# Optimization experiments

Measured on AMD Instinct MI355X. Metric: run time of the kernel, lower is better.

## Reference

```python
import jax, jax.numpy as jnp
import numpy as np

NUM_CLASSES = 21
THRESHOLD = 0.5
NEGPOS_RATIO = 3
VAR0, VAR1 = 0.1, 0.2


def setup_inputs() -> dict:
    key = jax.random.key(0)
    k1, k2, k3, k4, k5, k6, k7 = jax.random.split(key, 7)
    N, P, M = 64, 24564, 16
    loc_data = jax.random.normal(k1, (N, P, 4), dtype=jnp.float32)
    conf_data = jax.random.normal(k2, (N, P, NUM_CLASSES), dtype=jnp.float32)
    # priors in center form (cx, cy, w, h), all inside the unit square
    pc = jax.random.uniform(k3, (P, 2)) * 0.9 + 0.05
    pwh = jax.random.uniform(k4, (P, 2)) * 0.2 + 0.02
    priors = jnp.concatenate([pc, pwh], axis=-1).astype(jnp.float32)
    # ground truth boxes in corner form (xmin, ymin, xmax, ymax, label)
    tc = jax.random.uniform(k5, (N, M, 2)) * 0.8 + 0.1
    twh = jax.random.uniform(k6, (N, M, 2)) * 0.2 + 0.05
    lab = jax.random.randint(k7, (N, M, 1), 0, NUM_CLASSES - 1).astype(jnp.float32)
    targets = jnp.concatenate([tc - twh / 2, tc + twh / 2, lab], axis=-1)
    return {"loc_data": loc_data, "conf_data": conf_data, "priors": priors, "targets": targets}


def _point_form(p):  # center form -> corner form
    return jnp.concatenate([p[:, :2] - p[:, 2:] / 2, p[:, :2] + p[:, 2:] / 2], axis=-1)


def _jaccard(a, b):  # a: [M,4] corner, b: [P,4] corner -> [M,P]
    max_xy = jnp.minimum(a[:, None, 2:], b[None, :, 2:])
    min_xy = jnp.maximum(a[:, None, :2], b[None, :, :2])
    inter = jnp.clip(max_xy - min_xy, 0.0).prod(-1)
    area_a = ((a[:, 2] - a[:, 0]) * (a[:, 3] - a[:, 1]))[:, None]
    area_b = ((b[:, 2] - b[:, 0]) * (b[:, 3] - b[:, 1]))[None, :]
    return inter / (area_a + area_b - inter)


def _encode(matched, priors):  # matched corner form [P,4], priors center form [P,4]
    g_cxcy = ((matched[:, :2] + matched[:, 2:]) / 2 - priors[:, :2]) / (VAR0 * priors[:, 2:])
    g_wh = jnp.log((matched[:, 2:] - matched[:, :2]) / priors[:, 2:]) / VAR1
    return jnp.concatenate([g_cxcy, g_wh], axis=-1)


def _match(truth, label, priors):  # truth [M,4], label [M], priors [P,4]
    overlaps = _jaccard(truth, _point_form(priors))        # [M,P]
    best_prior_idx = jnp.argmax(overlaps, axis=1)          # [M]
    best_truth_idx = jnp.argmax(overlaps, axis=0)          # [P]
    best_truth_ov = overlaps.max(axis=0)                   # [P]
    # ensure every gt matches its best prior
    best_truth_ov = best_truth_ov.at[best_prior_idx].set(2.0)
    best_truth_idx = best_truth_idx.at[best_prior_idx].set(jnp.arange(truth.shape[0]))
    matched = truth[best_truth_idx]                        # [P,4]
    conf = (label[best_truth_idx] + 1).astype(jnp.int32)
    conf = jnp.where(best_truth_ov < THRESHOLD, 0, conf)
    return _encode(matched, priors), conf


def _multibox_loss(loc_data, conf_data, priors, targets):
    truths, labels = targets[..., :4], targets[..., 4]
    loc_t, conf_t = jax.vmap(_match, in_axes=(0, 0, None))(truths, labels, priors)
    pos = conf_t > 0                                        # [N,P]

    # localization: smooth-L1, summed over positive priors
    diff = loc_data - loc_t
    adiff = jnp.abs(diff)
    sl1 = jnp.where(adiff < 1.0, 0.5 * diff * diff, adiff - 0.5)
    loss_l = jnp.sum(sl1 * pos[..., None].astype(sl1.dtype))

    # per-prior softmax CE loss for hard negative mining
    lse = jax.scipy.special.logsumexp(conf_data, axis=-1)   # [N,P]
    gathered = jnp.take_along_axis(conf_data, conf_t[..., None], axis=-1)[..., 0]
    loss_c_all = lse - gathered                             # [N,P]
    loss_c_mined = jnp.where(pos, 0.0, loss_c_all)
    loss_idx = jnp.argsort(-loss_c_mined, axis=1)
    idx_rank = jnp.argsort(loss_idx, axis=1)                # rank of each prior by loss
    num_pos = pos.sum(axis=1, keepdims=True)                # [N,1]
    num_neg = jnp.minimum(NEGPOS_RATIO * num_pos, pos.shape[1] - 1)
    neg = idx_rank < num_neg
    sel = pos | neg
    loss_c = jnp.sum(jnp.where(sel, loss_c_all, 0.0))

    n = num_pos.sum().astype(jnp.float32)
    return loss_l / n, loss_c / n


def reference(loc_data, conf_data, priors, targets):
    return _multibox_loss(loc_data, conf_data, priors, targets)
```

## Files before the change

### kernel.cpp

```cpp
#include <hip/hip_runtime.h>
#include <math.h>

constexpr int N = 64;
constexpr int P = 24564;
constexpr int M = 16;
constexpr int C = 21;
constexpr float THRESH = 0.5f;

constexpr size_t OFF_SLL  = 0;
constexpr size_t OFF_SPOS = OFF_SLL + (size_t)N * 4;
constexpr size_t OFF_NP   = OFF_SPOS + (size_t)N * 4;
constexpr size_t OFF_BPK  = ((OFF_NP + (size_t)N * 4 + 15) / 16) * 16;
constexpr size_t OFF_ZEND = OFF_BPK + (size_t)N * M * 8;
constexpr size_t OFF_LCROW = ((OFF_ZEND + 15) / 16) * 16;
constexpr size_t OFF_MINED = ((OFF_LCROW + (size_t)N * 4 + 15) / 16) * 16;
constexpr size_t WS_NEEDED = OFF_MINED + (size_t)N * P * 4;

__device__ __forceinline__ float smooth_l1(float d) {
    float a = fabsf(d);
    return (a < 1.0f) ? 0.5f * d * d : (a - 0.5f);
}

__global__ __launch_bounds__(256) void k_match(
    const float* __restrict__ priors, const float* __restrict__ targets,
    unsigned long long* __restrict__ bpk) {
    const int n = blockIdx.y;
    const int tid = threadIdx.x;
    const int p = blockIdx.x * 256 + tid;
    __shared__ float st[M * 5];
    __shared__ unsigned int sbp_ov[M];
    __shared__ unsigned int sbp_idx[M];
    if (tid < M * 5) st[tid] = targets[(size_t)n * M * 5 + tid];
    if (tid < M) { sbp_ov[tid] = 0u; sbp_idx[tid] = 0xFFFFFFFFu; }
    __syncthreads();

    const bool active = p < P;
    float ovs[M];
    if (active) {
        float4 pr = reinterpret_cast<const float4*>(priors)[p];
        float bx1 = pr.x - pr.z * 0.5f, by1 = pr.y - pr.w * 0.5f;
        float bx2 = pr.x + pr.z * 0.5f, by2 = pr.y + pr.w * 0.5f;
        float area_b = (bx2 - bx1) * (by2 - by1);
        #pragma unroll
        for (int m = 0; m < M; ++m) {
            float tx1 = st[m * 5 + 0], ty1 = st[m * 5 + 1];
            float tx2 = st[m * 5 + 2], ty2 = st[m * 5 + 3];
            float ix = fmaxf(fminf(tx2, bx2) - fmaxf(tx1, bx1), 0.0f);
            float iy = fmaxf(fminf(ty2, by2) - fmaxf(ty1, by1), 0.0f);
            float inter = ix * iy;
            float area_a = (tx2 - tx1) * (ty2 - ty1);
            float ov = inter / (area_a + area_b - inter);
            ovs[m] = ov;
            unsigned int bits = __float_as_uint(ov);
            if (bits > sbp_ov[m]) atomicMax(&sbp_ov[m], bits);
        }
    }
    __syncthreads();
    if (active) {
        #pragma unroll
        for (int m = 0; m < M; ++m) {
            if (__float_as_uint(ovs[m]) == sbp_ov[m])
                atomicMin(&sbp_idx[m], (unsigned)p);
        }
    }
    __syncthreads();
    if (tid < M) {
        unsigned long long key =
            ((unsigned long long)sbp_ov[tid] << 32) |
            (unsigned long long)(0xFFFFFFFFu - sbp_idx[tid]);
        unsigned long long* dst = &bpk[(size_t)n * M + tid];
        if (key > *dst) atomicMax(dst, key);
    }
}

__global__ __launch_bounds__(256) void k_loss(
    const float* __restrict__ loc, const float* __restrict__ conf,
    const float* __restrict__ priors, const float* __restrict__ targets,
    const unsigned long long* __restrict__ bpk,
    float* __restrict__ mined, float* __restrict__ s_ll,
    int* __restrict__ num_pos, float* __restrict__ s_pos) {
    const int n = blockIdx.y;
    const int p0 = blockIdx.x * 256;
    const int tid = threadIdx.x;
    __shared__ __align__(16) float sc[256 * C];
    __shared__ float st[M * 5];
    __shared__ unsigned int fprior[M];
    __shared__ float wll[4], wsp[4];
    __shared__ int wnp[4];

    {
        const float4* src4 = reinterpret_cast<const float4*>(
            conf + (size_t)n * P * C + (size_t)p0 * C);
        float4* sc4 = reinterpret_cast<float4*>(sc);
        int cnt4 = (min(256, P - p0) * C) >> 2;
        for (int i = tid; i < cnt4; i += 256) sc4[i] = src4[i];
    }
    if (tid < M * 5) st[tid] = targets[(size_t)n * M * 5 + tid];
    if (tid < M)
        fprior[tid] = 0xFFFFFFFFu -
                      (unsigned int)(bpk[(size_t)n * M + tid] & 0xFFFFFFFFull);
    __syncthreads();

    float my_ll = 0.0f, my_sp = 0.0f;
    int my_np = 0;
    const int p = p0 + tid;
    if (p < P) {
        float4 pr = reinterpret_cast<const float4*>(priors)[p];
        float bx1 = pr.x - pr.z * 0.5f, by1 = pr.y - pr.w * 0.5f;
        float bx2 = pr.x + pr.z * 0.5f, by2 = pr.y + pr.w * 0.5f;
        float area_b = (bx2 - bx1) * (by2 - by1);
        float bestv = -1.0f;
        int bestm = 0;
        #pragma unroll
        for (int m = 0; m < M; ++m) {
            float tx1 = st[m * 5 + 0], ty1 = st[m * 5 + 1];
            float tx2 = st[m * 5 + 2], ty2 = st[m * 5 + 3];
            float ix = fmaxf(fminf(tx2, bx2) - fmaxf(tx1, bx1), 0.0f);
            float iy = fmaxf(fminf(ty2, by2) - fmaxf(ty1, by1), 0.0f);
            float inter = ix * iy;
            float area_a = (tx2 - tx1) * (ty2 - ty1);
            float ov = inter / (area_a + area_b - inter);
            if (ov > bestv) { bestv = ov; bestm = m; }
        }
        #pragma unroll
        for (int m = 0; m < M; ++m) {
            if (fprior[m] == (unsigned)p) { bestv = 2.0f; bestm = m; }
        }
        bool pos = !(bestv < THRESH);
        float mx1 = st[bestm * 5 + 0], my1 = st[bestm * 5 + 1];
        float mx2 = st[bestm * 5 + 2], my2 = st[bestm * 5 + 3];
        int conf_t = pos ? ((int)st[bestm * 5 + 4] + 1) : 0;

        if (pos) {
            float gcx = ((mx1 + mx2) * 0.5f - pr.x) / (0.1f * pr.z);
            float gcy = ((my1 + my2) * 0.5f - pr.y) / (0.1f * pr.w);
            float gw = logf((mx2 - mx1) / pr.z) / 0.2f;
            float gh = logf((my2 - my1) / pr.w) / 0.2f;
            float4 ld = reinterpret_cast<const float4*>(loc)[(size_t)n * P + p];
            my_ll = smooth_l1(ld.x - gcx) + smooth_l1(ld.y - gcy) +
                    smooth_l1(ld.z - gw) + smooth_l1(ld.w - gh);
            my_np = 1;
        }
        float cv[C];
        #pragma unroll
        for (int c = 0; c < C; ++c) cv[c] = sc[tid * C + c];
        float mx = cv[0];
        #pragma unroll
        for (int c = 1; c < C; ++c) mx = fmaxf(mx, cv[c]);
        float s = 0.0f;
        #pragma unroll
        for (int c = 0; c < C; ++c) s += expf(cv[c] - mx);
        float gathered = sc[tid * C + conf_t];
        float lc = mx + logf(s) - gathered;
        if (pos) my_sp = lc;
        mined[(size_t)n * P + p] = pos ? 0.0f : lc;
    }

    for (int off = 32; off > 0; off >>= 1) {
        my_ll += __shfl_down(my_ll, off);
        my_sp += __shfl_down(my_sp, off);
        my_np += __shfl_down(my_np, off);
    }
    int wave = tid >> 6, lane = tid & 63;
    if (lane == 0) { wll[wave] = my_ll; wsp[wave] = my_sp; wnp[wave] = my_np; }
    __syncthreads();
    if (tid == 0) {
        float ll = wll[0] + wll[1] + wll[2] + wll[3];
        float sp = wsp[0] + wsp[1] + wsp[2] + wsp[3];
        int np_ = wnp[0] + wnp[1] + wnp[2] + wnp[3];
        if (ll != 0.0f) atomicAdd(&s_ll[n], ll);
        if (np_) atomicAdd(&num_pos[n], np_);
        if (sp != 0.0f) atomicAdd(&s_pos[n], sp);
    }
}

__global__ __launch_bounds__(1024) void k_select(
    const float* __restrict__ mined, const int* __restrict__ num_pos,
    const float* __restrict__ s_pos, float* __restrict__ lcrow) {
    const int n = blockIdx.x;
    const int tid = threadIdx.x;
    const int wid = tid >> 6, lane = tid & 63;
    const float4* row4 = reinterpret_cast<const float4*>(mined + (size_t)n * P);
    constexpr int P4 = P / 4;

    __shared__ unsigned int whist[16 * 256];
    __shared__ unsigned int hist[256];
    __shared__ unsigned int suf[256];
    __shared__ unsigned int s_prefix;
    __shared__ int s_remK;
    __shared__ float wsg[16];
    __shared__ int wcg[16];

    const int K = min(3 * num_pos[n], P - 1);
    if (K <= 0) {
        if (tid == 0) lcrow[n] = s_pos[n];
        return;
    }

    unsigned int prefix = 0;
    int remK = K;
    for (int pass = 0; pass < 4; ++pass) {
        const int shift = 24 - pass * 8;
        const unsigned int himask = (pass == 0) ? 0u : (0xFFFFFFFFu << (shift + 8));
        for (int i = tid; i < 16 * 256; i += 1024) whist[i] = 0;
        __syncthreads();
        unsigned int* mh = &whist[wid * 256];
        for (int i = tid; i < P4; i += 1024) {
            float4 v = row4[i];
            unsigned int k0 = __float_as_uint(v.x), k1 = __float_as_uint(v.y);
            unsigned int k2 = __float_as_uint(v.z), k3 = __float_as_uint(v.w);
            if ((k0 & himask) == prefix) atomicAdd(&mh[(k0 >> shift) & 255u], 1u);
            if ((k1 & himask) == prefix) atomicAdd(&mh[(k1 >> shift) & 255u], 1u);
            if ((k2 & himask) == prefix) atomicAdd(&mh[(k2 >> shift) & 255u], 1u);
            if ((k3 & himask) == prefix) atomicAdd(&mh[(k3 >> shift) & 255u], 1u);
        }
        __syncthreads();
        if (tid < 256) {
            unsigned int h = 0;
            #pragma unroll
            for (int w = 0; w < 16; ++w) h += whist[w * 256 + tid];
            hist[tid] = h;
        }
        __syncthreads();
        if (tid < 64) {
            unsigned int h0 = hist[tid * 4 + 0], h1 = hist[tid * 4 + 1];
            unsigned int h2 = hist[tid * 4 + 2], h3 = hist[tid * 4 + 3];
            unsigned int s3 = h3, s2 = h2 + s3, s1 = h1 + s2, s0 = h0 + s1;
            unsigned int tot = s0;
            #pragma unroll
            for (int off = 1; off < 64; off <<= 1) {
                unsigned int v = __shfl_down(tot, off);
                if (lane + off < 64) tot += v;
            }
            unsigned int above = tot - s0;
            suf[tid * 4 + 0] = above + s0;
            suf[tid * 4 + 1] = above + s1;
            suf[tid * 4 + 2] = above + s2;
            suf[tid * 4 + 3] = above + s3;
        }
        __syncthreads();
        if (tid < 256) {
            unsigned int Sb = suf[tid];
            unsigned int Sb1 = (tid == 255) ? 0u : suf[tid + 1];
            if (Sb >= (unsigned)remK && Sb1 < (unsigned)remK) {
                s_prefix = prefix | ((unsigned)tid << shift);
                s_remK = remK - (int)Sb1;
            }
        }
        __syncthreads();
        prefix = s_prefix;
        remK = s_remK;
        __syncthreads();
    }
    const float T = __uint_as_float(prefix);
    float sgt = 0.0f;
    int cgt = 0;
    for (int i = tid; i < P4; i += 1024) {
        float4 v = row4[i];
        if (v.x > T) { sgt += v.x; cgt++; }
        if (v.y > T) { sgt += v.y; cgt++; }
        if (v.z > T) { sgt += v.z; cgt++; }
        if (v.w > T) { sgt += v.w; cgt++; }
    }
    for (int off = 32; off > 0; off >>= 1) {
        sgt += __shfl_down(sgt, off);
        cgt += __shfl_down(cgt, off);
    }
    if (lane == 0) { wsg[wid] = sgt; wcg[wid] = cgt; }
    __syncthreads();
    if (tid == 0) {
        float S = 0.0f;
        int Cg = 0;
        #pragma unroll
        for (int w = 0; w < 16; ++w) { S += wsg[w]; Cg += wcg[w]; }
        lcrow[n] = s_pos[n] + S + (float)(K - Cg) * T;
    }
}

__global__ void k_final(const float* __restrict__ s_ll,
                        const int* __restrict__ num_pos,
                        const float* __restrict__ lcrow,
                        float* __restrict__ out) {
    int t = threadIdx.x;
    float llv = s_ll[t];
    int npv = num_pos[t];
    float lcv = lcrow[t];
    for (int off = 32; off > 0; off >>= 1) {
        llv += __shfl_down(llv, off);
        npv += __shfl_down(npv, off);
        lcv += __shfl_down(lcv, off);
    }
    if (t == 0) {
        float nf = (float)npv;
        out[0] = llv / nf;
        out[1] = lcv / nf;
    }
}

extern "C" void kernel_launch(void* const* d_in, const int* in_sizes, int n_in,
                              void* d_out, int out_size, void* d_ws, size_t ws_size,
                              hipStream_t stream) {
    const float* loc = (const float*)d_in[0];
    const float* conf = (const float*)d_in[1];
    const float* priors = (const float*)d_in[2];
    const float* targets = (const float*)d_in[3];

    if (ws_size < WS_NEEDED) return;

    char* ws = (char*)d_ws;
    float* s_ll = (float*)(ws + OFF_SLL);
    float* s_pos = (float*)(ws + OFF_SPOS);
    int* num_pos = (int*)(ws + OFF_NP);
    unsigned long long* bpk = (unsigned long long*)(ws + OFF_BPK);
    float* lcrow = (float*)(ws + OFF_LCROW);
    float* mined = (float*)(ws + OFF_MINED);

    hipMemsetAsync(ws, 0, OFF_ZEND, stream);

    dim3 grid((P + 255) / 256, N);
    k_match<<<grid, 256, 0, stream>>>(priors, targets, bpk);
    k_loss<<<grid, 256, 0, stream>>>(loc, conf, priors, targets, bpk,
                                     mined, s_ll, num_pos, s_pos);
    k_select<<<N, 1024, 0, stream>>>(mined, num_pos, s_pos, lcrow);
    k_final<<<1, 64, 0, stream>>>(s_ll, num_pos, lcrow, (float*)d_out);
}
```

Measured before the change: 318.0 us.

## Use wave-sized blocks, wave-level argmax, fast math, and two-stage candidate radix select

```diff
diff --git a/kernel.cpp b/kernel.cpp
--- a/kernel.cpp
+++ b/kernel.cpp
@@ -5,7 +5,6 @@
 constexpr int P = 24564;
 constexpr int M = 16;
 constexpr int C = 21;
-constexpr float THRESH = 0.5f;
 
 constexpr size_t OFF_SLL  = 0;
 constexpr size_t OFF_SPOS = OFF_SLL + (size_t)N * 4;
@@ -21,90 +20,76 @@
     return (a < 1.0f) ? 0.5f * d * d : (a - 0.5f);
 }
 
-__global__ __launch_bounds__(256) void k_match(
+__global__ __launch_bounds__(64) void k_match(
     const float* __restrict__ priors, const float* __restrict__ targets,
     unsigned long long* __restrict__ bpk) {
     const int n = blockIdx.y;
-    const int tid = threadIdx.x;
-    const int p = blockIdx.x * 256 + tid;
-    __shared__ float st[M * 5];
-    __shared__ unsigned int sbp_ov[M];
-    __shared__ unsigned int sbp_idx[M];
-    if (tid < M * 5) st[tid] = targets[(size_t)n * M * 5 + tid];
-    if (tid < M) { sbp_ov[tid] = 0u; sbp_idx[tid] = 0xFFFFFFFFu; }
-    __syncthreads();
-
+    const int lane = threadIdx.x;
+    const int p = blockIdx.x * 64 + lane;
     const bool active = p < P;
-    float ovs[M];
-    if (active) {
-        float4 pr = reinterpret_cast<const float4*>(priors)[p];
-        float bx1 = pr.x - pr.z * 0.5f, by1 = pr.y - pr.w * 0.5f;
-        float bx2 = pr.x + pr.z * 0.5f, by2 = pr.y + pr.w * 0.5f;
-        float area_b = (bx2 - bx1) * (by2 - by1);
-        #pragma unroll
-        for (int m = 0; m < M; ++m) {
-            float tx1 = st[m * 5 + 0], ty1 = st[m * 5 + 1];
-            float tx2 = st[m * 5 + 2], ty2 = st[m * 5 + 3];
-            float ix = fmaxf(fminf(tx2, bx2) - fmaxf(tx1, bx1), 0.0f);
-            float iy = fmaxf(fminf(ty2, by2) - fmaxf(ty1, by1), 0.0f);
-            float inter = ix * iy;
-            float area_a = (tx2 - tx1) * (ty2 - ty1);
-            float ov = inter / (area_a + area_b - inter);
-            ovs[m] = ov;
-            unsigned int bits = __float_as_uint(ov);
-            if (bits > sbp_ov[m]) atomicMax(&sbp_ov[m], bits);
-        }
-    }
-    __syncthreads();
-    if (active) {
-        #pragma unroll
-        for (int m = 0; m < M; ++m) {
-            if (__float_as_uint(ovs[m]) == sbp_ov[m])
-                atomicMin(&sbp_idx[m], (unsigned)p);
-        }
-    }
-    __syncthreads();
-    if (tid < M) {
-        unsigned long long key =
-            ((unsigned long long)sbp_ov[tid] << 32) |
-            (unsigned long long)(0xFFFFFFFFu - sbp_idx[tid]);
-        unsigned long long* dst = &bpk[(size_t)n * M + tid];
-        if (key > *dst) atomicMax(dst, key);
-    }
-}
-
-__global__ __launch_bounds__(256) void k_loss(
+    const float* tgt = targets + (size_t)n * M * 5;
+    const unsigned long long* bpk_row = bpk + (size_t)n * M;
+
+    float4 pr = reinterpret_cast<const float4*>(priors)[active ? p : (P - 1)];
+    float bx1 = pr.x - pr.z * 0.5f, by1 = pr.y - pr.w * 0.5f;
+    float bx2 = pr.x + pr.z * 0.5f, by2 = pr.y + pr.w * 0.5f;
+    float area_b = (bx2 - bx1) * (by2 - by1);
+
+    #pragma unroll
+    for (int m = 0; m < M; ++m) {
+        const float tx1 = tgt[m * 5 + 0], ty1 = tgt[m * 5 + 1];
+        const float tx2 = tgt[m * 5 + 2], ty2 = tgt[m * 5 + 3];
+        float ix = fmaxf(fminf(tx2, bx2) - fmaxf(tx1, bx1), 0.0f);
+        float iy = fmaxf(fminf(ty2, by2) - fmaxf(ty1, by1), 0.0f);
+        float inter = ix * iy;
+        float area_a = (tx2 - tx1) * (ty2 - ty1);
+        float ov = inter * __builtin_amdgcn_rcpf(area_a + area_b - inter);
+        unsigned int bits = active ? __float_as_uint(ov) : 0u;
+        unsigned int wmax = bits;
+        #pragma unroll
+        for (int off = 1; off < 64; off <<= 1)
+            wmax = max(wmax, (unsigned int)__shfl_xor((int)wmax, off));
+        unsigned long long tied = __ballot(active && bits == wmax);
+        int leader = (int)__ffsll((unsigned long long)tied) - 1;
+        if (lane == leader) {
+            unsigned long long key =
+                ((unsigned long long)wmax << 32) |
+                (unsigned long long)(0xFFFFFFFFu - (unsigned)p);
+            unsigned long long* dst = (unsigned long long*)&bpk_row[m];
+            if (key > *dst) atomicMax(dst, key);
+        }
+    }
+}
+
+__global__ __launch_bounds__(64) void k_loss(
     const float* __restrict__ loc, const float* __restrict__ conf,
     const float* __restrict__ priors, const float* __restrict__ targets,
     const unsigned long long* __restrict__ bpk,
     float* __restrict__ mined, float* __restrict__ s_ll,
     int* __restrict__ num_pos, float* __restrict__ s_pos) {
     const int n = blockIdx.y;
-    const int p0 = blockIdx.x * 256;
-    const int tid = threadIdx.x;
-    __shared__ __align__(16) float sc[256 * C];
+    const int p0 = blockIdx.x * 64;
+    const int lane = threadIdx.x;
+    const int p = p0 + lane;
+    const bool active = p < P;
+    __shared__ __align__(16) float sc[64 * C];
     __shared__ float st[M * 5];
-    __shared__ unsigned int fprior[M];
-    __shared__ float wll[4], wsp[4];
-    __shared__ int wnp[4];
+    const float* tgt = targets + (size_t)n * M * 5;
+    const unsigned long long* bpk_row = bpk + (size_t)n * M;
 
     {
         const float4* src4 = reinterpret_cast<const float4*>(
             conf + (size_t)n * P * C + (size_t)p0 * C);
         float4* sc4 = reinterpret_cast<float4*>(sc);
-        int cnt4 = (min(256, P - p0) * C) >> 2;
-        for (int i = tid; i < cnt4; i += 256) sc4[i] = src4[i];
-    }
-    if (tid < M * 5) st[tid] = targets[(size_t)n * M * 5 + tid];
-    if (tid < M)
-        fprior[tid] = 0xFFFFFFFFu -
-                      (unsigned int)(bpk[(size_t)n * M + tid] & 0xFFFFFFFFull);
+        int cnt4 = (min(64, P - p0) * C) >> 2;
+        for (int i = lane; i < cnt4; i += 64) sc4[i] = src4[i];
+    }
+    for (int i = lane; i < M * 5; i += 64) st[i] = tgt[i];
     __syncthreads();
 
     float my_ll = 0.0f, my_sp = 0.0f;
     int my_np = 0;
-    const int p = p0 + tid;
-    if (p < P) {
+    if (active) {
         float4 pr = reinterpret_cast<const float4*>(priors)[p];
         float bx1 = pr.x - pr.z * 0.5f, by1 = pr.y - pr.w * 0.5f;
         float bx2 = pr.x + pr.z * 0.5f, by2 = pr.y + pr.w * 0.5f;
@@ -113,45 +98,40 @@
         int bestm = 0;
         #pragma unroll
         for (int m = 0; m < M; ++m) {
-            float tx1 = st[m * 5 + 0], ty1 = st[m * 5 + 1];
-            float tx2 = st[m * 5 + 2], ty2 = st[m * 5 + 3];
+            const float tx1 = tgt[m * 5 + 0], ty1 = tgt[m * 5 + 1];
+            const float tx2 = tgt[m * 5 + 2], ty2 = tgt[m * 5 + 3];
             float ix = fmaxf(fminf(tx2, bx2) - fmaxf(tx1, bx1), 0.0f);
             float iy = fmaxf(fminf(ty2, by2) - fmaxf(ty1, by1), 0.0f);
             float inter = ix * iy;
             float area_a = (tx2 - tx1) * (ty2 - ty1);
-            float ov = inter / (area_a + area_b - inter);
+            float ov = inter * __builtin_amdgcn_rcpf(area_a + area_b - inter);
             if (ov > bestv) { bestv = ov; bestm = m; }
         }
         #pragma unroll
         for (int m = 0; m < M; ++m) {
-            if (fprior[m] == (unsigned)p) { bestv = 2.0f; bestm = m; }
-        }
-        bool pos = !(bestv < THRESH);
-        float mx1 = st[bestm * 5 + 0], my1 = st[bestm * 5 + 1];
-        float mx2 = st[bestm * 5 + 2], my2 = st[bestm * 5 + 3];
-        int conf_t = pos ? ((int)st[bestm * 5 + 4] + 1) : 0;
-
+            unsigned int fp = 0xFFFFFFFFu -
+                              (unsigned int)(bpk_row[m] & 0xFFFFFFFFull);
+            if (fp == (unsigned)p) { bestv = 2.0f; bestm = m; }
+        }
+        bool pos = !(bestv < 0.5f);
+        int conf_t = 0;
         if (pos) {
+            float mx1 = st[bestm * 5 + 0], my1 = st[bestm * 5 + 1];
+            float mx2 = st[bestm * 5 + 2], my2 = st[bestm * 5 + 3];
+            conf_t = (int)st[bestm * 5 + 4] + 1;
             float gcx = ((mx1 + mx2) * 0.5f - pr.x) / (0.1f * pr.z);
             float gcy = ((my1 + my2) * 0.5f - pr.y) / (0.1f * pr.w);
-            float gw = logf((mx2 - mx1) / pr.z) / 0.2f;
-            float gh = logf((my2 - my1) / pr.w) / 0.2f;
+            float gw = __logf((mx2 - mx1) / pr.z) * 5.0f;
+            float gh = __logf((my2 - my1) / pr.w) * 5.0f;
             float4 ld = reinterpret_cast<const float4*>(loc)[(size_t)n * P + p];
             my_ll = smooth_l1(ld.x - gcx) + smooth_l1(ld.y - gcy) +
                     smooth_l1(ld.z - gw) + smooth_l1(ld.w - gh);
             my_np = 1;
         }
-        float cv[C];
-        #pragma unroll
-        for (int c = 0; c < C; ++c) cv[c] = sc[tid * C + c];
-        float mx = cv[0];
-        #pragma unroll
-        for (int c = 1; c < C; ++c) mx = fmaxf(mx, cv[c]);
         float s = 0.0f;
         #pragma unroll
-        for (int c = 0; c < C; ++c) s += expf(cv[c] - mx);
-        float gathered = sc[tid * C + conf_t];
-        float lc = mx + logf(s) - gathered;
+        for (int c = 0; c < C; ++c) s += __expf(sc[lane * C + c]);
+        float lc = __logf(s) - sc[lane * C + conf_t];
         if (pos) my_sp = lc;
         mined[(size_t)n * P + p] = pos ? 0.0f : lc;
     }
@@ -161,19 +141,14 @@
         my_sp += __shfl_down(my_sp, off);
         my_np += __shfl_down(my_np, off);
     }
-    int wave = tid >> 6, lane = tid & 63;
-    if (lane == 0) { wll[wave] = my_ll; wsp[wave] = my_sp; wnp[wave] = my_np; }
-    __syncthreads();
-    if (tid == 0) {
-        float ll = wll[0] + wll[1] + wll[2] + wll[3];
-        float sp = wsp[0] + wsp[1] + wsp[2] + wsp[3];
-        int np_ = wnp[0] + wnp[1] + wnp[2] + wnp[3];
-        if (ll != 0.0f) atomicAdd(&s_ll[n], ll);
-        if (np_) atomicAdd(&num_pos[n], np_);
-        if (sp != 0.0f) atomicAdd(&s_pos[n], sp);
-    }
-}
-
+    if (lane == 0) {
+        if (my_ll != 0.0f) atomicAdd(&s_ll[n], my_ll);
+        if (my_np) atomicAdd(&num_pos[n], my_np);
+        if (my_sp != 0.0f) atomicAdd(&s_pos[n], my_sp);
+    }
+}
+
+constexpr int CAP = 11264;
 __global__ __launch_bounds__(1024) void k_select(
     const float* __restrict__ mined, const int* __restrict__ num_pos,
     const float* __restrict__ s_pos, float* __restrict__ lcrow) {
@@ -183,13 +158,14 @@
     const float4* row4 = reinterpret_cast<const float4*>(mined + (size_t)n * P);
     constexpr int P4 = P / 4;
 
-    __shared__ unsigned int whist[16 * 256];
-    __shared__ unsigned int hist[256];
-    __shared__ unsigned int suf[256];
-    __shared__ unsigned int s_prefix;
-    __shared__ int s_remK;
-    __shared__ float wsg[16];
-    __shared__ int wcg[16];
+    __shared__ unsigned int hist[2][2048];
+    __shared__ unsigned int cand[CAP];
+    __shared__ unsigned int hist2[128];
+    __shared__ unsigned int wtot[16], sabove[16];
+    __shared__ float sred[16];
+    __shared__ unsigned int credu[16];
+    __shared__ int s_b0, s_remK, s_cc;
+    __shared__ unsigned int s_pref;
 
     const int K = min(3 * num_pos[n], P - 1);
     if (K <= 0) {
@@ -197,83 +173,164 @@
         return;
     }
 
-    unsigned int prefix = 0;
-    int remK = K;
-    for (int pass = 0; pass < 4; ++pass) {
-        const int shift = 24 - pass * 8;
-        const unsigned int himask = (pass == 0) ? 0u : (0xFFFFFFFFu << (shift + 8));
-        for (int i = tid; i < 16 * 256; i += 1024) whist[i] = 0;
-        __syncthreads();
-        unsigned int* mh = &whist[wid * 256];
+    for (int i = tid; i < 2 * 2048; i += 1024) ((unsigned int*)hist)[i] = 0;
+    if (tid == 0) s_cc = 0;
+    __syncthreads();
+    {
+        unsigned int* mh = hist[wid & 1];
         for (int i = tid; i < P4; i += 1024) {
             float4 v = row4[i];
-            unsigned int k0 = __float_as_uint(v.x), k1 = __float_as_uint(v.y);
-            unsigned int k2 = __float_as_uint(v.z), k3 = __float_as_uint(v.w);
-            if ((k0 & himask) == prefix) atomicAdd(&mh[(k0 >> shift) & 255u], 1u);
-            if ((k1 & himask) == prefix) atomicAdd(&mh[(k1 >> shift) & 255u], 1u);
-            if ((k2 & himask) == prefix) atomicAdd(&mh[(k2 >> shift) & 255u], 1u);
-            if ((k3 & himask) == prefix) atomicAdd(&mh[(k3 >> shift) & 255u], 1u);
-        }
-        __syncthreads();
-        if (tid < 256) {
-            unsigned int h = 0;
+            atomicAdd(&mh[__float_as_uint(v.x) >> 21], 1u);
+            atomicAdd(&mh[__float_as_uint(v.y) >> 21], 1u);
+            atomicAdd(&mh[__float_as_uint(v.z) >> 21], 1u);
+            atomicAdd(&mh[__float_as_uint(v.w) >> 21], 1u);
+        }
+    }
+    __syncthreads();
+    {
+        unsigned int h0 = hist[0][2 * tid] + hist[1][2 * tid];
+        unsigned int h1 = hist[0][2 * tid + 1] + hist[1][2 * tid + 1];
+        unsigned int pt = h0 + h1;
+        unsigned int x = pt;
+        #pragma unroll
+        for (int off = 1; off < 64; off <<= 1) {
+            unsigned int v = (unsigned int)__shfl_down((int)x, off);
+            if (lane + off < 64) x += v;
+        }
+        if (lane == 0) wtot[wid] = x;
+        __syncthreads();
+        if (tid < 16) {
+            unsigned int y = wtot[tid];
             #pragma unroll
-            for (int w = 0; w < 16; ++w) h += whist[w * 256 + tid];
-            hist[tid] = h;
+            for (int off = 1; off < 16; off <<= 1) {
+                unsigned int v = (unsigned int)__shfl_down((int)y, off);
+                if (tid + off < 16) y += v;
+            }
+            sabove[tid] = y - wtot[tid];
+        }
+        __syncthreads();
+        unsigned int pairsuf = x + sabove[wid];
+        unsigned int uk = (unsigned)K;
+        if (pairsuf >= uk && pairsuf - h0 < uk) {
+            s_b0 = 2 * tid;
+            s_remK = K - (int)(pairsuf - h0);
+        }
+        if (pairsuf - h0 >= uk && pairsuf - pt < uk) {
+            s_b0 = 2 * tid + 1;
+            s_remK = K - (int)(pairsuf - pt);
+        }
+    }
+    __syncthreads();
+    const int b0 = s_b0;
+    const unsigned int ncand = hist[0][b0] + hist[1][b0];
+    const bool ok = ncand <= (unsigned)CAP;
+
+    float sgt = 0.0f;
+    unsigned int cgt = 0;
+    for (int i = tid; i < P4; i += 1024) {
+        float4 v = row4[i];
+        float fv[4] = {v.x, v.y, v.z, v.w};
+        #pragma unroll
+        for (int c = 0; c < 4; ++c) {
+            unsigned int bits = __float_as_uint(fv[c]);
+            int bin = (int)(bits >> 21);
+            if (bin > b0) { sgt += fv[c]; cgt++; }
+            bool isc = ok && (bin == b0);
+            unsigned long long mb = __ballot(isc);
+            if (isc) {
+                int ldr = (int)__ffsll(mb) - 1;
+                int base = 0;
+                if (lane == ldr) base = atomicAdd(&s_cc, (int)__popcll(mb));
+                base = __shfl(base, ldr);
+                int rank = (int)__popcll(mb & ((1ull << lane) - 1ull));
+                cand[base + rank] = bits;
+            }
+        }
+    }
+    __syncthreads();
+    const int nc = s_cc;
+
+    if (tid == 0) s_pref = ((unsigned int)b0) << 21;
+    __syncthreads();
+    const unsigned int pmasks[3] = {0xFFE00000u, 0xFFFFC000u, 0xFFFFFF80u};
+    const int shifts[3] = {14, 7, 0};
+    for (int pass = 0; pass < 3; ++pass) {
+        const unsigned int pmask = pmasks[pass];
+        const int sh = shifts[pass];
+        const unsigned int pref = s_pref;
+        const int remK = s_remK;
+        if (tid < 128) hist2[tid] = 0;
+        __syncthreads();
+        if (ok) {
+            for (int i = tid; i < nc; i += 1024) {
+                unsigned int b = cand[i];
+                if ((b & pmask) == pref) atomicAdd(&hist2[(b >> sh) & 127u], 1u);
+            }
+        } else {
+            for (int i = tid; i < P4; i += 1024) {
+                float4 v = row4[i];
+                unsigned int bb[4] = {__float_as_uint(v.x), __float_as_uint(v.y),
+                                      __float_as_uint(v.z), __float_as_uint(v.w)};
+                #pragma unroll
+                for (int c = 0; c < 4; ++c)
+                    if ((bb[c] & pmask) == pref)
+                        atomicAdd(&hist2[(bb[c] >> sh) & 127u], 1u);
+            }
         }
         __syncthreads();
         if (tid < 64) {
-            unsigned int h0 = hist[tid * 4 + 0], h1 = hist[tid * 4 + 1];
-            unsigned int h2 = hist[tid * 4 + 2], h3 = hist[tid * 4 + 3];
-            unsigned int s3 = h3, s2 = h2 + s3, s1 = h1 + s2, s0 = h0 + s1;
-            unsigned int tot = s0;
+            unsigned int g0 = hist2[2 * tid], g1 = hist2[2 * tid + 1];
+            unsigned int gt = g0 + g1;
+            unsigned int y = gt;
             #pragma unroll
             for (int off = 1; off < 64; off <<= 1) {
-                unsigned int v = __shfl_down(tot, off);
-                if (lane + off < 64) tot += v;
-            }
-            unsigned int above = tot - s0;
-            suf[tid * 4 + 0] = above + s0;
-            suf[tid * 4 + 1] = above + s1;
-            suf[tid * 4 + 2] = above + s2;
-            suf[tid * 4 + 3] = above + s3;
-        }
-        __syncthreads();
-        if (tid < 256) {
-            unsigned int Sb = suf[tid];
-            unsigned int Sb1 = (tid == 255) ? 0u : suf[tid + 1];
-            if (Sb >= (unsigned)remK && Sb1 < (unsigned)remK) {
-                s_prefix = prefix | ((unsigned)tid << shift);
-                s_remK = remK - (int)Sb1;
-            }
-        }
-        __syncthreads();
-        prefix = s_prefix;
-        remK = s_remK;
-        __syncthreads();
-    }
-    const float T = __uint_as_float(prefix);
-    float sgt = 0.0f;
-    int cgt = 0;
-    for (int i = tid; i < P4; i += 1024) {
-        float4 v = row4[i];
-        if (v.x > T) { sgt += v.x; cgt++; }
-        if (v.y > T) { sgt += v.y; cgt++; }
-        if (v.z > T) { sgt += v.z; cgt++; }
-        if (v.w > T) { sgt += v.w; cgt++; }
-    }
+                unsigned int v = (unsigned int)__shfl_down((int)y, off);
+                if (lane + off < 64) y += v;
+            }
+            unsigned int rk = (unsigned)remK;
+            if (y >= rk && y - g0 < rk) {
+                s_pref = pref | ((unsigned)(2 * tid) << sh);
+                s_remK = remK - (int)(y - g0);
+            }
+            if (y - g0 >= rk && y - gt < rk) {
+                s_pref = pref | ((unsigned)(2 * tid + 1) << sh);
+                s_remK = remK - (int)(y - gt);
+            }
+        }
+        __syncthreads();
+    }
+    const unsigned int Tbits = s_pref;
+    const float T = __uint_as_float(Tbits);
+
+    if (ok) {
+        for (int i = tid; i < nc; i += 1024) {
+            unsigned int b = cand[i];
+            if (b > Tbits) { sgt += __uint_as_float(b); cgt++; }
+        }
+    } else {
+        for (int i = tid; i < P4; i += 1024) {
+            float4 v = row4[i];
+            float fv[4] = {v.x, v.y, v.z, v.w};
+            #pragma unroll
+            for (int c = 0; c < 4; ++c) {
+                unsigned int bits = __float_as_uint(fv[c]);
+                if ((int)(bits >> 21) == b0 && bits > Tbits) { sgt += fv[c]; cgt++; }
+            }
+        }
+    }
+
     for (int off = 32; off > 0; off >>= 1) {
         sgt += __shfl_down(sgt, off);
-        cgt += __shfl_down(cgt, off);
-    }
-    if (lane == 0) { wsg[wid] = sgt; wcg[wid] = cgt; }
+        cgt += (unsigned int)__shfl_down((int)cgt, off);
+    }
+    if (lane == 0) { sred[wid] = sgt; credu[wid] = cgt; }
     __syncthreads();
     if (tid == 0) {
         float S = 0.0f;
-        int Cg = 0;
-        #pragma unroll
-        for (int w = 0; w < 16; ++w) { S += wsg[w]; Cg += wcg[w]; }
-        lcrow[n] = s_pos[n] + S + (float)(K - Cg) * T;
+        unsigned int Cg = 0;
+        #pragma unroll
+        for (int w = 0; w < 16; ++w) { S += sred[w]; Cg += credu[w]; }
+        lcrow[n] = s_pos[n] + S + (float)(K - (int)Cg) * T;
     }
 }
 
@@ -317,10 +374,10 @@
 
     hipMemsetAsync(ws, 0, OFF_ZEND, stream);
 
-    dim3 grid((P + 255) / 256, N);
-    k_match<<<grid, 256, 0, stream>>>(priors, targets, bpk);
-    k_loss<<<grid, 256, 0, stream>>>(loc, conf, priors, targets, bpk,
-                                     mined, s_ll, num_pos, s_pos);
+    dim3 grid((P + 63) / 64, N);
+    k_match<<<grid, 64, 0, stream>>>(priors, targets, bpk);
+    k_loss<<<grid, 64, 0, stream>>>(loc, conf, priors, targets, bpk,
+                                    mined, s_ll, num_pos, s_pos);
     k_select<<<N, 1024, 0, stream>>>(mined, num_pos, s_pos, lcrow);
     k_final<<<1, 64, 0, stream>>>(s_ll, num_pos, lcrow, (float*)d_out);
 }
```

Measured after the change: 692.1 us. 2.18x slower.
